# Performance work log

Measured on AMD Instinct MI355X. Metric: run time of the kernel, lower is better.

## Reference

```python
import jax, jax.numpy as jnp
import numpy as np

N_NODES = 100000
N_EDGES = 1600000
N_GRAPHS = 1000
HID = 128
NCLS = 3


def setup_inputs() -> dict:
    key = jax.random.key(0)
    ks = jax.random.split(key, 16)
    x = jax.random.normal(ks[0], (N_NODES, 1), dtype=jnp.float32)
    edge_index = jax.random.randint(ks[1], (2, N_EDGES), 0, N_NODES, dtype=jnp.int64)
    edge_attr = jax.random.normal(ks[2], (N_EDGES, 1), dtype=jnp.float32)
    batch = jnp.sort(jax.random.randint(ks[3], (N_NODES,), 0, N_GRAPHS, dtype=jnp.int64))
    s1 = 1.0 / np.sqrt(1.0)
    sh = 1.0 / np.sqrt(HID)
    # layer 0 MLP: 1 -> HID -> HID
    W1_0 = jax.random.uniform(ks[4], (1, HID), minval=-s1, maxval=s1)
    b1_0 = jax.random.uniform(ks[5], (HID,), minval=-s1, maxval=s1)
    W2_0 = jax.random.uniform(ks[6], (HID, HID), minval=-sh, maxval=sh)
    b2_0 = jax.random.uniform(ks[7], (HID,), minval=-sh, maxval=sh)
    # layers 1..3 MLPs stacked: HID -> HID -> HID
    W1_s = jax.random.uniform(ks[8], (3, HID, HID), minval=-sh, maxval=sh)
    b1_s = jax.random.uniform(ks[9], (3, HID), minval=-sh, maxval=sh)
    W2_s = jax.random.uniform(ks[10], (3, HID, HID), minval=-sh, maxval=sh)
    b2_s = jax.random.uniform(ks[11], (3, HID), minval=-sh, maxval=sh)
    Wc = jax.random.uniform(ks[12], (HID, NCLS), minval=-sh, maxval=sh)
    bc = jax.random.uniform(ks[13], (NCLS,), minval=-sh, maxval=sh)
    return {"x": x, "edge_index": edge_index, "edge_attr": edge_attr, "batch": batch,
            "W1_0": W1_0, "b1_0": b1_0, "W2_0": W2_0, "b2_0": b2_0,
            "W1_s": W1_s, "b1_s": b1_s, "W2_s": W2_s, "b2_s": b2_s,
            "Wc": Wc, "bc": bc}


def _gine_layer(x, src, dst, edge_attr, W1, b1, W2, b2):
    # message: ReLU(x_j + e_ji), broadcast over feature dim ([E,1] edge_attr)
    msg = jax.nn.relu(x[src] + edge_attr)                       # [E, F]
    agg = jax.ops.segment_sum(msg, dst, num_segments=x.shape[0])  # [N, F]
    h = x + agg                                                 # (1 + eps)*x + agg, eps = 0
    return jax.nn.relu(h @ W1 + b1) @ W2 + b2                   # MLP


def reference(x, edge_index, edge_attr, batch,
              W1_0, b1_0, W2_0, b2_0, W1_s, b1_s, W2_s, b2_s, Wc, bc):
    src, dst = edge_index[0], edge_index[1]
    h = jax.nn.relu(_gine_layer(x, src, dst, edge_attr, W1_0, b1_0, W2_0, b2_0))
    for i in range(3):
        h = jax.nn.relu(_gine_layer(h, src, dst, edge_attr,
                                    W1_s[i], b1_s[i], W2_s[i], b2_s[i]))
    # global mean pool per graph
    summed = jax.ops.segment_sum(h, batch, num_segments=N_GRAPHS)       # [G, HID]
    counts = jax.ops.segment_sum(jnp.ones((h.shape[0],), h.dtype), batch,
                                 num_segments=N_GRAPHS)                  # [G]
    pooled = summed / jnp.maximum(counts, 1.0)[:, None]
    return pooled @ Wc + bc                                              # [G, NCLS]
```

## Files before the change

### kernel.cpp

```cpp
#include <hip/hip_runtime.h>
#include <hip/hip_bf16.h>


#define HID 128
#define NCLS 3
#define EPB 8192
#define BSHIFT 8
#define BNODES 256
#define ECAP 5504

typedef _Float16 f16;
typedef f16 f16x2 __attribute__((ext_vector_type(2)));
typedef f16 f16x8 __attribute__((ext_vector_type(8)));
typedef float f32x2 __attribute__((ext_vector_type(2)));
typedef float f32x4 __attribute__((ext_vector_type(4)));
typedef unsigned short ushort;

__device__ __forceinline__ float bcf(int v) {
    return __builtin_bit_cast(float, v);
}
__device__ __forceinline__ float f16bits2f(ushort u) {
    return (float)__builtin_bit_cast(f16, u);
}


__global__ __launch_bounds__(1024) void k_bin2(const int* __restrict__ src,
                                               const int* __restrict__ dst,
                                               const float* __restrict__ eattr,
                                               const float* __restrict__ x,
                                               int* __restrict__ cursor,
                                               int2* __restrict__ ebuf,
                                               int E, int NB) {
    __shared__ int lh[512];
    __shared__ int lbase[512];
    __shared__ int lrsv[512];
    int t = threadIdx.x;
    if (t < NB) lh[t] = 0;
    __syncthreads();
    int base = blockIdx.x * EPB;
    int myd[8];
    #pragma unroll
    for (int j = 0; j < 8; ++j) {
        int e = base + j * 1024 + t;
        myd[j] = (e < E) ? dst[e] : -1;
        if (myd[j] >= 0) atomicAdd(&lh[myd[j] >> BSHIFT], 1);
    }
    __syncthreads();
    if (t < NB) {
        int c = lh[t];
        int cp = (c + 7) & ~7;
        lrsv[t] = cp;
        lbase[t] = (cp > 0) ? (t * ECAP + atomicAdd(&cursor[t], cp)) : 0;
        lh[t] = 0;
    }
    __syncthreads();
    #pragma unroll
    for (int j = 0; j < 8; ++j) {
        if (myd[j] >= 0) {
            int e = base + j * 1024 + t;
            int b = myd[j] >> BSHIFT;
            int s = src[e];
            float at = eattr[e];
            float msg = fmaxf(x[s] + at, 0.f);
            unsigned a16 = __builtin_bit_cast(ushort, (f16)at);
            unsigned m16 = __builtin_bit_cast(ushort, (f16)msg);
            int r = atomicAdd(&lh[b], 1);
            int pos = lbase[b] + r;
            if (pos < (b + 1) * ECAP)
                ebuf[pos] = make_int2(s | ((myd[j] & (BNODES - 1)) << 24),
                                      (int)((a16 << 16) | m16));
        }
    }
    __syncthreads();
    if (t < NB) {
        int c = lh[t], cp = lrsv[t];
        int p0 = lbase[t] + c;
        int pe = lbase[t] + cp;
        int cap = (t + 1) * ECAP;
        if (pe > cap) pe = cap;
        for (int pos = p0; pos < pe; ++pos)
            ebuf[pos] = make_int2(-1, 0);
    }
}


__global__ __launch_bounds__(1024) void k_prep(const float* __restrict__ W2_0,
                                               const float* __restrict__ W1_s,
                                               const float* __restrict__ W2_s,
                                               f16* __restrict__ Wf,
                                               const int* __restrict__ cursor,
                                               int* __restrict__ bbase, int NB) {
    int t = threadIdx.x;
    if (blockIdx.x < 14) {
        int id = blockIdx.x * 1024 + t;
        int lane = id & 63;
        int w    = (id >> 6) & 3;
        int nf   = (id >> 8) & 1;
        int kk   = (id >> 9) & 3;
        int g    = id >> 11;
        const float* W = (g == 0) ? W2_0
                       : ((g & 1) ? W1_s + (size_t)((g - 1) >> 1) * HID * HID
                                  : W2_s + (size_t)((g - 2) >> 1) * HID * HID);
        int col = w * 32 + nf * 16 + (lane & 15);
        int k0  = kk * 32 + (lane >> 4) * 8;
        f16x8 hi;
        #pragma unroll
        for (int j = 0; j < 8; ++j)
            hi[j] = (f16)W[(k0 + j) * HID + col];
        size_t o = ((((size_t)g * 4 + kk) * 2 + nf) * 4 + w) * 512 +
                   (size_t)lane * 8;
        *(f16x8*)&Wf[o] = hi;
    } else {
        __shared__ int sd[1024];
        int v = (t < NB) ? min(cursor[t], ECAP) : 0;
        sd[t] = v;
        __syncthreads();
        #pragma unroll
        for (int o = 1; o < 1024; o <<= 1) {
            int add = (t >= o) ? sd[t - o] : 0;
            __syncthreads();
            sd[t] += add;
            __syncthreads();
        }
        if (t < NB) bbase[t] = sd[t] - v;
        if (t == 1023) bbase[NB] = sd[1023];
    }
}

__global__ __launch_bounds__(512, 8) void k_fill2(const int2* __restrict__ ebuf,
                                               const int* __restrict__ btot,
                                               const int* __restrict__ bbase,
                                               const float* __restrict__ x,
                                               const int* __restrict__ batch,
                                               int2* __restrict__ meta,
                                               int2* __restrict__ pairs,
                                               float* __restrict__ hin0,
                                               int* __restrict__ gcount,
                                               int* __restrict__ gstart,
                                               int N) {
    __shared__ int lcnt[BNODES];
    __shared__ int lofs[BNODES];
    __shared__ float satom[BNODES];
    int b = blockIdx.x, t = threadIdx.x;
    int estart = b * ECAP;
    int cnt = min(btot[b], ECAP);
    int pstart = bbase[b];
    int nb0 = b << BSHIFT;
    if (t < BNODES) {
        lcnt[t] = 0;
        satom[t] = 0.f;
        int node = nb0 + t;
        if (node < N) {
            int gb = batch[node];
            atomicAdd(&gcount[gb], 1);
            if (node == 0 || batch[node - 1] != gb) gstart[gb] = node;
        }
    }
    __syncthreads();
    int2 myv[11];
    #pragma unroll
    for (int j = 0; j < 11; ++j) {
        int i = j * 512 + t;
        if (i < cnt) myv[j] = ebuf[estart + i];
    }
    #pragma unroll
    for (int j = 0; j < 11; ++j) {
        int i = j * 512 + t;
        if (i < cnt && myv[j].x != -1)
            atomicAdd(&lcnt[((unsigned)myv[j].x) >> 24], 1);
    }
    __syncthreads();
    if (t < 64) {
        int c0 = lcnt[4 * t], c1 = lcnt[4 * t + 1];
        int c2 = lcnt[4 * t + 2], c3 = lcnt[4 * t + 3];
        int s = c0 + c1 + c2 + c3;
        int sa = s;
        #pragma unroll
        for (int o = 1; o < 64; o <<= 1) {
            int v = __shfl_up(sa, o);
            if (t >= o) sa += v;
        }
        int e0 = sa - s;
        int e1 = e0 + c0, e2 = e1 + c1, e3 = e2 + c2;
        lofs[4 * t] = e0; lofs[4 * t + 1] = e1;
        lofs[4 * t + 2] = e2; lofs[4 * t + 3] = e3;
        lcnt[4 * t] = 0; lcnt[4 * t + 1] = 0;
        lcnt[4 * t + 2] = 0; lcnt[4 * t + 3] = 0;
        int n0 = nb0 + 4 * t;
        if (n0 < N)     meta[n0]     = make_int2(pstart + e0, c0);
        if (n0 + 1 < N) meta[n0 + 1] = make_int2(pstart + e1, c1);
        if (n0 + 2 < N) meta[n0 + 2] = make_int2(pstart + e2, c2);
        if (n0 + 3 < N) meta[n0 + 3] = make_int2(pstart + e3, c3);
    }
    __syncthreads();
    #pragma unroll
    for (int j = 0; j < 11; ++j) {
        int i = j * 512 + t;
        if (i < cnt) {
            int2 v = myv[j];
            if (v.x != -1) {
                int ld = ((unsigned)v.x) >> 24;
                int srcid = v.x & 0x00FFFFFF;
                ushort a16 = (ushort)(((unsigned)v.y) >> 16);
                ushort m16 = (ushort)(v.y & 0xFFFF);
                int r = atomicAdd(&lcnt[ld], 1);
                int pos = lofs[ld] + r;
                pairs[pstart + pos] = make_int2(srcid << 7,
                                     __builtin_bit_cast(int, f16bits2f(a16)));
                atomicAdd(&satom[ld], f16bits2f(m16));
            }
        }
    }
    __syncthreads();
    if (t < BNODES) {
        int node = nb0 + t;
        if (node < N) hin0[node] = x[node] + satom[t];
    }
}


__device__ __forceinline__ void agg_add8(f32x2 acc2[4], uint2 g, float e) {
    f32x2 e2 = {e, e}, z2 = {0.f, 0.f};
    unsigned gw[2] = {g.x, g.y};
    #pragma unroll
    for (int ww = 0; ww < 2; ++ww) {
        f32x2 lo = __builtin_amdgcn_cvt_pk_f32_fp8((int)gw[ww], false);
        f32x2 hi = __builtin_amdgcn_cvt_pk_f32_fp8((int)gw[ww], true);
        lo = __builtin_elementwise_max(lo + e2, z2);
        hi = __builtin_elementwise_max(hi + e2, z2);
        acc2[2 * ww]     += lo;
        acc2[2 * ww + 1] += hi;
    }
}

__device__ __forceinline__ uint2 agg_ld8(const char* __restrict__ hb,
                                         int voff) {
    return *(const uint2*)(hb + (unsigned)voff);
}

__global__ __launch_bounds__(256, 4) void k_agg(
    const unsigned char* __restrict__ h8,
    const f16* __restrict__ hf,
    const int2* __restrict__ pairs,
    const int2* __restrict__ meta,
    f16* __restrict__ oh, int n) {

    int t = threadIdx.x;
    int w = t >> 6, lane = t & 63;
    int g = lane >> 4, c = lane & 15;
    int node = blockIdx.x * 16 + w * 4 + g;
    int c8 = c * 8;
    int sbase = g * 16;
    const char* hb = (const char*)h8;

    int2 m = make_int2(0, 0);
    if (node < n) m = meta[node];
    int off = m.x, d = m.y;
    f32x2 acc2[4] = {{0.f,0.f},{0.f,0.f},{0.f,0.f},{0.f,0.f}};

    for (int wb = 0; wb < d; wb += 16) {
        int rem = d - wb;
        int mm = rem < 16 ? rem : 16;
        int2 pr = make_int2(0, 0);
        if (c < mm) pr = pairs[off + wb + c];
        uint2 gg[16];
        #pragma unroll
        for (int p = 0; p < 16; ++p) {
            int s = __shfl(pr.x, sbase + p);
            if (p < mm) gg[p] = agg_ld8(hb, s + c8);
        }
        #pragma unroll
        for (int p = 0; p < 16; ++p) {
            if (p < mm) {
                float e = bcf(__shfl(pr.y, sbase + p));
                agg_add8(acc2, gg[p], e);
            }
        }
    }

    if (node < n) {
        uint4 sg = *(const uint4*)&hf[(size_t)node * HID + c8];
        unsigned sw[4] = {sg.x, sg.y, sg.z, sg.w};
        unsigned ow[4];
        #pragma unroll
        for (int ww = 0; ww < 4; ++ww) {
            f16x2 s = __builtin_bit_cast(f16x2, sw[ww]);
            f16x2 o;
            o[0] = (f16)((float)s[0] + acc2[ww].x);
            o[1] = (f16)((float)s[1] + acc2[ww].y);
            ow[ww] = __builtin_bit_cast(unsigned, o);
        }
        uint4 o4;
        o4.x = ow[0]; o4.y = ow[1]; o4.z = ow[2]; o4.w = ow[3];
        *(uint4*)&oh[(size_t)node * HID + c8] = o4;
    }
}


__device__ __forceinline__ void load_wfrags1(const f16* __restrict__ Wfg,
                                             int w, int lane,
                                             f16x8 whf[4][2]) {
    #pragma unroll
    for (int kk = 0; kk < 4; ++kk)
        #pragma unroll
        for (int nf = 0; nf < 2; ++nf) {
            size_t o = (((size_t)kk * 2 + nf) * 4 + w) * 512 +
                       (size_t)lane * 8;
            whf[kk][nf] = *(const f16x8*)&Wfg[o];
        }
}

__device__ __forceinline__ void do_gemm1(const f16* Ah,
                                         const f16x8 whf[4][2],
                                         int lane, f32x4 acc[4][2]) {
    int arow = lane & 15, akgrp = lane >> 4;
    #pragma unroll
    for (int kk = 0; kk < 4; ++kk) {
        int chunk = kk * 4 + akgrp;
        f16x8 ah[4];
        #pragma unroll
        for (int mf = 0; mf < 4; ++mf) {
            int r = mf * 16 + arow;
            int swz = chunk ^ (r & 15);
            ah[mf] = *(const f16x8*)&Ah[r * HID + swz * 8];
        }
        #pragma unroll
        for (int mf = 0; mf < 4; ++mf)
            #pragma unroll
            for (int nf = 0; nf < 2; ++nf)
                acc[mf][nf] = __builtin_amdgcn_mfma_f32_16x16x32_f16(
                    ah[mf], whf[kk][nf], acc[mf][nf], 0, 0, 0);
    }
}


__global__ __launch_bounds__(256, 3) void k_mlp(
    const f16* __restrict__ A_g,
    const f16* __restrict__ Wf1, const float* __restrict__ b1,
    const f16* __restrict__ Wf2, const float* __restrict__ b2,
    f16* __restrict__ O, unsigned char* __restrict__ O8, int w8, int n) {

    __shared__ __align__(16) f16 bufA[64 * HID];
    int t = threadIdx.x, w = t >> 6, lane = t & 63;
    int wcol = w * 32, fcol = lane & 15, kgrp = lane >> 4;
    int row0 = blockIdx.x * 64;

    #pragma unroll
    for (int rep = 0; rep < 4; ++rep) {
        int task = rep * 256 + t;
        int r = task >> 4, ch = task & 15;
        int gr = min(row0 + r, n - 1);
        int swz = ch ^ (r & 15);
        *(f16x8*)&bufA[r * HID + swz * 8] =
            *(const f16x8*)&A_g[(size_t)gr * HID + ch * 8];
    }

    f32x4 acc[4][2];
    {
        f16x8 whf[4][2];
        load_wfrags1(Wf1, w, lane, whf);
        float bv0 = b1[wcol + fcol], bv1 = b1[wcol + 16 + fcol];
        __syncthreads();
        #pragma unroll
        for (int mf = 0; mf < 4; ++mf)
            #pragma unroll
            for (int nf = 0; nf < 2; ++nf)
                acc[mf][nf] = (f32x4)(0.f);
        do_gemm1(bufA, whf, lane, acc);
        __syncthreads();
        #pragma unroll
        for (int mf = 0; mf < 4; ++mf)
            #pragma unroll
            for (int nf = 0; nf < 2; ++nf) {
                int cc = wcol + nf * 16 + fcol;
                float bb = nf ? bv1 : bv0;
                #pragma unroll
                for (int j = 0; j < 4; ++j) {
                    int r = mf * 16 + kgrp * 4 + j;
                    float v = fmaxf(acc[mf][nf][j] + bb, 0.f);
                    int addr = r * HID + (((cc >> 3) ^ (r & 15)) << 3) + (cc & 7);
                    bufA[addr] = (f16)v;
                }
            }
    }
    {
        f16x8 whf[4][2];
        load_wfrags1(Wf2, w, lane, whf);
        float bv0 = b2[wcol + fcol], bv1 = b2[wcol + 16 + fcol];
        __syncthreads();
        #pragma unroll
        for (int mf = 0; mf < 4; ++mf)
            #pragma unroll
            for (int nf = 0; nf < 2; ++nf)
                acc[mf][nf] = (f32x4)(0.f);
        do_gemm1(bufA, whf, lane, acc);

        #pragma unroll
        for (int mf = 0; mf < 4; ++mf)
            #pragma unroll
            for (int nf = 0; nf < 2; ++nf) {
                int cc = wcol + nf * 16 + fcol;
                float bb = nf ? bv1 : bv0;
                #pragma unroll
                for (int j = 0; j < 4; ++j) {
                    int r = row0 + mf * 16 + kgrp * 4 + j;
                    if (r < n) {
                        float v = fmaxf(acc[mf][nf][j] + bb, 0.f);
                        O[(size_t)r * HID + cc] = (f16)v;
                        if (w8) {
                            int pk = __builtin_amdgcn_cvt_pk_fp8_f32(
                                v, v, 0, false);
                            O8[(size_t)r * HID + cc] =
                                (unsigned char)(pk & 0xFF);
                        }
                    }
                }
            }
    }
}


__global__ __launch_bounds__(256, 3) void k_mlp0(
    const float* __restrict__ r1x, const float* __restrict__ r1w,
    const float* __restrict__ r1b,
    const f16* __restrict__ Wf2, const float* __restrict__ b2,
    f16* __restrict__ O, unsigned char* __restrict__ O8, int n) {

    __shared__ __align__(16) f16 bufA[64 * HID];
    int t = threadIdx.x, w = t >> 6, lane = t & 63;
    int wcol = w * 32, fcol = lane & 15, kgrp = lane >> 4;
    int row0 = blockIdx.x * 64;

    #pragma unroll
    for (int rep = 0; rep < 4; ++rep) {
        int task = rep * 256 + t;
        int r = task >> 4, ch = task & 15;
        int gr = min(row0 + r, n - 1);
        int swz = ch ^ (r & 15);
        float xv = r1x[gr];
        f16x8 hi;
        #pragma unroll
        for (int j = 0; j < 8; ++j)
            hi[j] = (f16)fmaxf(xv * r1w[ch * 8 + j] + r1b[ch * 8 + j], 0.f);
        *(f16x8*)&bufA[r * HID + swz * 8] = hi;
    }

    f16x8 whf[4][2];
    load_wfrags1(Wf2, w, lane, whf);
    float bv0 = b2[wcol + fcol], bv1 = b2[wcol + 16 + fcol];
    __syncthreads();
    f32x4 acc[4][2];
    #pragma unroll
    for (int mf = 0; mf < 4; ++mf)
        #pragma unroll
        for (int nf = 0; nf < 2; ++nf)
            acc[mf][nf] = (f32x4)(0.f);
    do_gemm1(bufA, whf, lane, acc);

    #pragma unroll
    for (int mf = 0; mf < 4; ++mf)
        #pragma unroll
        for (int nf = 0; nf < 2; ++nf) {
            int cc = wcol + nf * 16 + fcol;
            float bb = nf ? bv1 : bv0;
            #pragma unroll
            for (int j = 0; j < 4; ++j) {
                int r = row0 + mf * 16 + kgrp * 4 + j;
                if (r < n) {
                    float v = fmaxf(acc[mf][nf][j] + bb, 0.f);
                    O[(size_t)r * HID + cc] = (f16)v;
                    int pk = __builtin_amdgcn_cvt_pk_fp8_f32(v, v, 0, false);
                    O8[(size_t)r * HID + cc] = (unsigned char)(pk & 0xFF);
                }
            }
        }
}


__global__ __launch_bounds__(256) void k_head(const f16* __restrict__ h,
                                              const int* __restrict__ gstart,
                                              const int* __restrict__ gcount,
                                              const float* __restrict__ Wc,
                                              const float* __restrict__ bc,
                                              float* __restrict__ out, int G) {
    __shared__ float2 red[4][64];
    __shared__ float pl[HID];
    int g = blockIdx.x, t = threadIdx.x;
    int rr = t >> 6, cc = t & 63;
    int st = gstart[g], c = gcount[g];
    float2 acc = make_float2(0.f, 0.f);
    for (int i = rr; i < c; i += 4) {
        unsigned u = *(const unsigned*)&h[(size_t)(st + i) * HID + cc * 2];
        f16x2 v = __builtin_bit_cast(f16x2, u);
        acc.x += (float)v[0];
        acc.y += (float)v[1];
    }
    red[rr][cc] = acc;
    __syncthreads();
    if (rr == 0) {
        #pragma unroll
        for (int k = 1; k < 4; ++k) {
            acc.x += red[k][cc].x;
            acc.y += red[k][cc].y;
        }
        float inv = 1.f / fmaxf((float)c, 1.f);
        pl[cc * 2]     = acc.x * inv;
        pl[cc * 2 + 1] = acc.y * inv;
    }
    __syncthreads();
    if (t < NCLS) {
        float o = bc[t];
        for (int k = 0; k < HID; ++k) o += pl[k] * Wc[k * NCLS + t];
        out[g * NCLS + t] = o;
    }
}


static inline size_t alignup(size_t x, size_t a) { return (x + a - 1) & ~(a - 1); }

extern "C" void kernel_launch(void* const* d_in, const int* in_sizes, int n_in,
                              void* d_out, int out_size, void* d_ws, size_t ws_size,
                              hipStream_t stream) {
    const float* x      = (const float*)d_in[0];
    const int*   ei     = (const int*)d_in[1];
    const float* eattr  = (const float*)d_in[2];
    const int*   batch  = (const int*)d_in[3];
    const float* W1_0   = (const float*)d_in[4];
    const float* b1_0   = (const float*)d_in[5];
    const float* W2_0   = (const float*)d_in[6];
    const float* b2_0   = (const float*)d_in[7];
    const float* W1_s   = (const float*)d_in[8];
    const float* b1_s   = (const float*)d_in[9];
    const float* W2_s   = (const float*)d_in[10];
    const float* b2_s   = (const float*)d_in[11];
    const float* Wc     = (const float*)d_in[12];
    const float* bc     = (const float*)d_in[13];

    const int N = in_sizes[0];
    const int E = in_sizes[2];
    const int G = out_size / NCLS;
    const int* srcI = ei;
    const int* dstI = ei + E;

    const int NB = (N + BNODES - 1) >> BSHIFT;
    const int NBLK = (E + EPB - 1) / EPB;

    char* p = (char*)d_ws;
    size_t off = 0;
    size_t gcount_off = off;         off = alignup(off + (size_t)G * 4, 256);
    size_t gstart_off = off;         off = alignup(off + (size_t)G * 4, 256);
    size_t cursor_off = off;         off = alignup(off + 512 * 4, 256);
    size_t zero_bytes = off;
    size_t meta_off = off;           off = alignup(off + (size_t)N * 8, 256);
    size_t bbase_off = off;          off = alignup(off + 513 * 4, 256);
    size_t hin0_off = off;           off = alignup(off + (size_t)N * 4, 256);
    size_t wf_off = off;             off = alignup(off + 7 * 16384 * 2, 256);
    size_t pairs_off = off;          off = alignup(off + (size_t)NB * ECAP * 8, 256);
    size_t p0_off = off;             off = alignup(off + (size_t)N * HID * 2, 256);
    size_t p8_off = off;             off = alignup(off + (size_t)N * HID, 256);
    size_t p1_off = off;             off = alignup(off + (size_t)N * HID * 2, 256);

    int*    gcount  = (int*)(p + gcount_off);
    int*    gstart  = (int*)(p + gstart_off);
    int*    cursor  = (int*)(p + cursor_off);
    int2*   meta    = (int2*)(p + meta_off);
    int*    bbase   = (int*)(p + bbase_off);
    float*  hin0    = (float*)(p + hin0_off);
    f16*    Wf      = (f16*)(p + wf_off);
    int2*   pairs   = (int2*)(p + pairs_off);
    f16*    P0      = (f16*)(p + p0_off);
    unsigned char* P8 = (unsigned char*)(p + p8_off);
    f16*    P1      = (f16*)(p + p1_off);
    int2*   ebuf    = (int2*)(p + p1_off);

    hipMemsetAsync(d_ws, 0, zero_bytes, stream);

    int gblk = (N + 63) / 64;
    int abl = (N + 15) / 16;

    k_bin2<<<NBLK, 1024, 0, stream>>>(srcI, dstI, eattr, x, cursor, ebuf,
                                      E, NB);
    k_prep<<<15, 1024, 0, stream>>>(W2_0, W1_s, W2_s, Wf, cursor, bbase, NB);
    k_fill2<<<NB, 512, 0, stream>>>(ebuf, cursor, bbase, x, batch, meta,
                                    pairs, hin0, gcount, gstart, N);

    #define WFG(g) (Wf + (size_t)(g) * 16384)

    k_mlp0<<<gblk, 256, 0, stream>>>(hin0, W1_0, b1_0, WFG(0), b2_0,
                                     P0, P8, N);

    for (int l = 0; l < 3; ++l) {
        const float* b1 = b1_s + (size_t)l * HID;
        const float* b2 = b2_s + (size_t)l * HID;
        k_agg<<<abl, 256, 0, stream>>>(P8, P0, pairs, meta, P1, N);
        k_mlp<<<gblk, 256, 0, stream>>>(P1, WFG(1 + 2 * l), b1,
                                        WFG(2 + 2 * l), b2, P0, P8,
                                        (l < 2) ? 1 : 0, N);
    }

    k_head<<<G, 256, 0, stream>>>(P0, gstart, gcount, Wc, bc,
                                  (float*)d_out, G);
}
```

Measured before the change: 308.6 us.

## Aggregate layer-0 messages with global atomics and fuse fill with first MLP

The binning kernel now accumulates the scalar layer-0 messages straight into a zeroed per-node fp32 buffer with global atomicAdd. It no longer packs fp16 message and attribute values into the edge buffer; the full fp32 edge attribute is stored instead. This removes the first MLP's dependency on the CSR fill pass. The fill kernel and the layer-0 MLP are merged into one launch with two kinds of blocks, so they can run concurrently and one launch is saved. In exchange it adds 1.6M contended global float atomics and makes the layer-0 sums order-nondeterministic.

```diff
diff --git a/kernel.cpp b/kernel.cpp
--- a/kernel.cpp
+++ b/kernel.cpp
@@ -19,9 +19,6 @@
 __device__ __forceinline__ float bcf(int v) {
     return __builtin_bit_cast(float, v);
 }
-__device__ __forceinline__ float f16bits2f(ushort u) {
-    return (float)__builtin_bit_cast(f16, u);
-}
 
 
 __global__ __launch_bounds__(1024) void k_bin2(const int* __restrict__ src,
@@ -29,6 +26,7 @@
                                                const float* __restrict__ eattr,
                                                const float* __restrict__ x,
                                                int* __restrict__ cursor,
+                                               float* __restrict__ agg0,
                                                int2* __restrict__ ebuf,
                                                int E, int NB) {
     __shared__ int lh[512];
@@ -62,13 +60,12 @@
             int s = src[e];
             float at = eattr[e];
             float msg = fmaxf(x[s] + at, 0.f);
-            unsigned a16 = __builtin_bit_cast(ushort, (f16)at);
-            unsigned m16 = __builtin_bit_cast(ushort, (f16)msg);
+            atomicAdd(&agg0[myd[j]], msg);
             int r = atomicAdd(&lh[b], 1);
             int pos = lbase[b] + r;
             if (pos < (b + 1) * ECAP)
                 ebuf[pos] = make_int2(s | ((myd[j] & (BNODES - 1)) << 24),
-                                      (int)((a16 << 16) | m16));
+                                      __builtin_bit_cast(int, at));
         }
     }
     __syncthreads();
@@ -127,94 +124,184 @@
     }
 }
 
-__global__ __launch_bounds__(512, 8) void k_fill2(const int2* __restrict__ ebuf,
-                                               const int* __restrict__ btot,
-                                               const int* __restrict__ bbase,
-                                               const float* __restrict__ x,
-                                               const int* __restrict__ batch,
-                                               int2* __restrict__ meta,
-                                               int2* __restrict__ pairs,
-                                               float* __restrict__ hin0,
-                                               int* __restrict__ gcount,
-                                               int* __restrict__ gstart,
-                                               int N) {
+
+__device__ __forceinline__ void load_wfrags1(const f16* __restrict__ Wfg,
+                                             int w, int lane,
+                                             f16x8 whf[4][2]) {
+    #pragma unroll
+    for (int kk = 0; kk < 4; ++kk)
+        #pragma unroll
+        for (int nf = 0; nf < 2; ++nf) {
+            size_t o = (((size_t)kk * 2 + nf) * 4 + w) * 512 +
+                       (size_t)lane * 8;
+            whf[kk][nf] = *(const f16x8*)&Wfg[o];
+        }
+}
+
+__device__ __forceinline__ void do_gemm1(const f16* Ah,
+                                         const f16x8 whf[4][2],
+                                         int lane, f32x4 acc[4][2]) {
+    int arow = lane & 15, akgrp = lane >> 4;
+    #pragma unroll
+    for (int kk = 0; kk < 4; ++kk) {
+        int chunk = kk * 4 + akgrp;
+        f16x8 ah[4];
+        #pragma unroll
+        for (int mf = 0; mf < 4; ++mf) {
+            int r = mf * 16 + arow;
+            int swz = chunk ^ (r & 15);
+            ah[mf] = *(const f16x8*)&Ah[r * HID + swz * 8];
+        }
+        #pragma unroll
+        for (int mf = 0; mf < 4; ++mf)
+            #pragma unroll
+            for (int nf = 0; nf < 2; ++nf)
+                acc[mf][nf] = __builtin_amdgcn_mfma_f32_16x16x32_f16(
+                    ah[mf], whf[kk][nf], acc[mf][nf], 0, 0, 0);
+    }
+}
+
+
+__global__ __launch_bounds__(512, 4) void k_fillm(
+    const int2* __restrict__ ebuf,
+    const int* __restrict__ btot,
+    const int* __restrict__ bbase,
+    const float* __restrict__ x,
+    const int* __restrict__ batch,
+    int2* __restrict__ meta,
+    int2* __restrict__ pairs,
+    const float* __restrict__ agg0,
+    int* __restrict__ gcount,
+    int* __restrict__ gstart,
+    const float* __restrict__ r1w, const float* __restrict__ r1b,
+    const f16* __restrict__ Wf2, const float* __restrict__ b2,
+    f16* __restrict__ O, unsigned char* __restrict__ O8,
+    int N, int NB) {
+
+    __shared__ __align__(16) f16 bufA2[2][64 * HID];
     __shared__ int lcnt[BNODES];
     __shared__ int lofs[BNODES];
-    __shared__ float satom[BNODES];
-    int b = blockIdx.x, t = threadIdx.x;
-    int estart = b * ECAP;
-    int cnt = min(btot[b], ECAP);
-    int pstart = bbase[b];
-    int nb0 = b << BSHIFT;
-    if (t < BNODES) {
-        lcnt[t] = 0;
-        satom[t] = 0.f;
-        int node = nb0 + t;
-        if (node < N) {
-            int gb = batch[node];
-            atomicAdd(&gcount[gb], 1);
-            if (node == 0 || batch[node - 1] != gb) gstart[gb] = node;
-        }
-    }
-    __syncthreads();
-    int2 myv[11];
-    #pragma unroll
-    for (int j = 0; j < 11; ++j) {
-        int i = j * 512 + t;
-        if (i < cnt) myv[j] = ebuf[estart + i];
-    }
-    #pragma unroll
-    for (int j = 0; j < 11; ++j) {
-        int i = j * 512 + t;
-        if (i < cnt && myv[j].x != -1)
-            atomicAdd(&lcnt[((unsigned)myv[j].x) >> 24], 1);
-    }
-    __syncthreads();
-    if (t < 64) {
-        int c0 = lcnt[4 * t], c1 = lcnt[4 * t + 1];
-        int c2 = lcnt[4 * t + 2], c3 = lcnt[4 * t + 3];
-        int s = c0 + c1 + c2 + c3;
-        int sa = s;
-        #pragma unroll
-        for (int o = 1; o < 64; o <<= 1) {
-            int v = __shfl_up(sa, o);
-            if (t >= o) sa += v;
-        }
-        int e0 = sa - s;
-        int e1 = e0 + c0, e2 = e1 + c1, e3 = e2 + c2;
-        lofs[4 * t] = e0; lofs[4 * t + 1] = e1;
-        lofs[4 * t + 2] = e2; lofs[4 * t + 3] = e3;
-        lcnt[4 * t] = 0; lcnt[4 * t + 1] = 0;
-        lcnt[4 * t + 2] = 0; lcnt[4 * t + 3] = 0;
-        int n0 = nb0 + 4 * t;
-        if (n0 < N)     meta[n0]     = make_int2(pstart + e0, c0);
-        if (n0 + 1 < N) meta[n0 + 1] = make_int2(pstart + e1, c1);
-        if (n0 + 2 < N) meta[n0 + 2] = make_int2(pstart + e2, c2);
-        if (n0 + 3 < N) meta[n0 + 3] = make_int2(pstart + e3, c3);
-    }
-    __syncthreads();
-    #pragma unroll
-    for (int j = 0; j < 11; ++j) {
-        int i = j * 512 + t;
-        if (i < cnt) {
-            int2 v = myv[j];
-            if (v.x != -1) {
-                int ld = ((unsigned)v.x) >> 24;
-                int srcid = v.x & 0x00FFFFFF;
-                ushort a16 = (ushort)(((unsigned)v.y) >> 16);
-                ushort m16 = (ushort)(v.y & 0xFFFF);
-                int r = atomicAdd(&lcnt[ld], 1);
-                int pos = lofs[ld] + r;
-                pairs[pstart + pos] = make_int2(srcid << 7,
-                                     __builtin_bit_cast(int, f16bits2f(a16)));
-                atomicAdd(&satom[ld], f16bits2f(m16));
-            }
-        }
-    }
-    __syncthreads();
-    if (t < BNODES) {
-        int node = nb0 + t;
-        if (node < N) hin0[node] = x[node] + satom[t];
+
+    if (blockIdx.x < NB) {
+        int b = blockIdx.x, t = threadIdx.x;
+        int estart = b * ECAP;
+        int cnt = min(btot[b], ECAP);
+        int pstart = bbase[b];
+        int nb0 = b << BSHIFT;
+        if (t < BNODES) {
+            lcnt[t] = 0;
+            int node = nb0 + t;
+            if (node < N) {
+                int gb = batch[node];
+                atomicAdd(&gcount[gb], 1);
+                if (node == 0 || batch[node - 1] != gb) gstart[gb] = node;
+            }
+        }
+        __syncthreads();
+        int2 myv[11];
+        #pragma unroll
+        for (int j = 0; j < 11; ++j) {
+            int i = j * 512 + t;
+            if (i < cnt) myv[j] = ebuf[estart + i];
+        }
+        #pragma unroll
+        for (int j = 0; j < 11; ++j) {
+            int i = j * 512 + t;
+            if (i < cnt && myv[j].x != -1)
+                atomicAdd(&lcnt[((unsigned)myv[j].x) >> 24], 1);
+        }
+        __syncthreads();
+        if (t < 64) {
+            int c0 = lcnt[4 * t], c1 = lcnt[4 * t + 1];
+            int c2 = lcnt[4 * t + 2], c3 = lcnt[4 * t + 3];
+            int s = c0 + c1 + c2 + c3;
+            int sa = s;
+            #pragma unroll
+            for (int o = 1; o < 64; o <<= 1) {
+                int v = __shfl_up(sa, o);
+                if (t >= o) sa += v;
+            }
+            int e0 = sa - s;
+            int e1 = e0 + c0, e2 = e1 + c1, e3 = e2 + c2;
+            lofs[4 * t] = e0; lofs[4 * t + 1] = e1;
+            lofs[4 * t + 2] = e2; lofs[4 * t + 3] = e3;
+            lcnt[4 * t] = 0; lcnt[4 * t + 1] = 0;
+            lcnt[4 * t + 2] = 0; lcnt[4 * t + 3] = 0;
+            int n0 = nb0 + 4 * t;
+            if (n0 < N)     meta[n0]     = make_int2(pstart + e0, c0);
+            if (n0 + 1 < N) meta[n0 + 1] = make_int2(pstart + e1, c1);
+            if (n0 + 2 < N) meta[n0 + 2] = make_int2(pstart + e2, c2);
+            if (n0 + 3 < N) meta[n0 + 3] = make_int2(pstart + e3, c3);
+        }
+        __syncthreads();
+        #pragma unroll
+        for (int j = 0; j < 11; ++j) {
+            int i = j * 512 + t;
+            if (i < cnt) {
+                int2 v = myv[j];
+                if (v.x != -1) {
+                    int ld = ((unsigned)v.x) >> 24;
+                    int srcid = v.x & 0x00FFFFFF;
+                    int r = atomicAdd(&lcnt[ld], 1);
+                    int pos = lofs[ld] + r;
+                    pairs[pstart + pos] = make_int2(srcid << 7, v.y);
+                }
+            }
+        }
+    } else {
+        int mb = blockIdx.x - NB;
+        int t = threadIdx.x;
+        int tile = t >> 8, tt = t & 255;
+        int w = tt >> 6, lane = tt & 63;
+        int wcol = w * 32, fcol = lane & 15, kgrp = lane >> 4;
+        int row0 = mb * 128 + tile * 64;
+        f16* bufA = &bufA2[tile][0];
+
+        #pragma unroll
+        for (int rep = 0; rep < 4; ++rep) {
+            int task = rep * 256 + tt;
+            int r = task >> 4, ch = task & 15;
+            int gr = min(row0 + r, N - 1);
+            int swz = ch ^ (r & 15);
+            float xv = x[gr] + agg0[gr];
+            f16x8 hi;
+            #pragma unroll
+            for (int j = 0; j < 8; ++j)
+                hi[j] = (f16)fmaxf(xv * r1w[ch * 8 + j] + r1b[ch * 8 + j],
+                                   0.f);
+            *(f16x8*)&bufA[r * HID + swz * 8] = hi;
+        }
+
+        f16x8 whf[4][2];
+        load_wfrags1(Wf2, w, lane, whf);
+        float bv0 = b2[wcol + fcol], bv1 = b2[wcol + 16 + fcol];
+        __syncthreads();
+        f32x4 acc[4][2];
+        #pragma unroll
+        for (int mf = 0; mf < 4; ++mf)
+            #pragma unroll
+            for (int nf = 0; nf < 2; ++nf)
+                acc[mf][nf] = (f32x4)(0.f);
+        do_gemm1(bufA, whf, lane, acc);
+
+        #pragma unroll
+        for (int mf = 0; mf < 4; ++mf)
+            #pragma unroll
+            for (int nf = 0; nf < 2; ++nf) {
+                int cc = wcol + nf * 16 + fcol;
+                float bb = nf ? bv1 : bv0;
+                #pragma unroll
+                for (int j = 0; j < 4; ++j) {
+                    int r = row0 + mf * 16 + kgrp * 4 + j;
+                    if (r < N) {
+                        float v = fmaxf(acc[mf][nf][j] + bb, 0.f);
+                        O[(size_t)r * HID + cc] = (f16)v;
+                        int pk = __builtin_amdgcn_cvt_pk_fp8_f32(v, v, 0,
+                                                                 false);
+                        O8[(size_t)r * HID + cc] = (unsigned char)(pk & 0xFF);
+                    }
+                }
+            }
     }
 }
 
@@ -293,43 +380,6 @@
         uint4 o4;
         o4.x = ow[0]; o4.y = ow[1]; o4.z = ow[2]; o4.w = ow[3];
         *(uint4*)&oh[(size_t)node * HID + c8] = o4;
-    }
-}
-
-
-__device__ __forceinline__ void load_wfrags1(const f16* __restrict__ Wfg,
-                                             int w, int lane,
-                                             f16x8 whf[4][2]) {
-    #pragma unroll
-    for (int kk = 0; kk < 4; ++kk)
-        #pragma unroll
-        for (int nf = 0; nf < 2; ++nf) {
-            size_t o = (((size_t)kk * 2 + nf) * 4 + w) * 512 +
-                       (size_t)lane * 8;
-            whf[kk][nf] = *(const f16x8*)&Wfg[o];
-        }
-}
-
-__device__ __forceinline__ void do_gemm1(const f16* Ah,
-                                         const f16x8 whf[4][2],
-                                         int lane, f32x4 acc[4][2]) {
-    int arow = lane & 15, akgrp = lane >> 4;
-    #pragma unroll
-    for (int kk = 0; kk < 4; ++kk) {
-        int chunk = kk * 4 + akgrp;
-        f16x8 ah[4];
-        #pragma unroll
-        for (int mf = 0; mf < 4; ++mf) {
-            int r = mf * 16 + arow;
-            int swz = chunk ^ (r & 15);
-            ah[mf] = *(const f16x8*)&Ah[r * HID + swz * 8];
-        }
-        #pragma unroll
-        for (int mf = 0; mf < 4; ++mf)
-            #pragma unroll
-            for (int nf = 0; nf < 2; ++nf)
-                acc[mf][nf] = __builtin_amdgcn_mfma_f32_16x16x32_f16(
-                    ah[mf], whf[kk][nf], acc[mf][nf], 0, 0, 0);
     }
 }
 
@@ -420,63 +470,6 @@
 }
 
 
-__global__ __launch_bounds__(256, 3) void k_mlp0(
-    const float* __restrict__ r1x, const float* __restrict__ r1w,
-    const float* __restrict__ r1b,
-    const f16* __restrict__ Wf2, const float* __restrict__ b2,
-    f16* __restrict__ O, unsigned char* __restrict__ O8, int n) {
-
-    __shared__ __align__(16) f16 bufA[64 * HID];
-    int t = threadIdx.x, w = t >> 6, lane = t & 63;
-    int wcol = w * 32, fcol = lane & 15, kgrp = lane >> 4;
-    int row0 = blockIdx.x * 64;
-
-    #pragma unroll
-    for (int rep = 0; rep < 4; ++rep) {
-        int task = rep * 256 + t;
-        int r = task >> 4, ch = task & 15;
-        int gr = min(row0 + r, n - 1);
-        int swz = ch ^ (r & 15);
-        float xv = r1x[gr];
-        f16x8 hi;
-        #pragma unroll
-        for (int j = 0; j < 8; ++j)
-            hi[j] = (f16)fmaxf(xv * r1w[ch * 8 + j] + r1b[ch * 8 + j], 0.f);
-        *(f16x8*)&bufA[r * HID + swz * 8] = hi;
-    }
-
-    f16x8 whf[4][2];
-    load_wfrags1(Wf2, w, lane, whf);
-    float bv0 = b2[wcol + fcol], bv1 = b2[wcol + 16 + fcol];
-    __syncthreads();
-    f32x4 acc[4][2];
-    #pragma unroll
-    for (int mf = 0; mf < 4; ++mf)
-        #pragma unroll
-        for (int nf = 0; nf < 2; ++nf)
-            acc[mf][nf] = (f32x4)(0.f);
-    do_gemm1(bufA, whf, lane, acc);
-
-    #pragma unroll
-    for (int mf = 0; mf < 4; ++mf)
-        #pragma unroll
-        for (int nf = 0; nf < 2; ++nf) {
-            int cc = wcol + nf * 16 + fcol;
-            float bb = nf ? bv1 : bv0;
-            #pragma unroll
-            for (int j = 0; j < 4; ++j) {
-                int r = row0 + mf * 16 + kgrp * 4 + j;
-                if (r < n) {
-                    float v = fmaxf(acc[mf][nf][j] + bb, 0.f);
-                    O[(size_t)r * HID + cc] = (f16)v;
-                    int pk = __builtin_amdgcn_cvt_pk_fp8_f32(v, v, 0, false);
-                    O8[(size_t)r * HID + cc] = (unsigned char)(pk & 0xFF);
-                }
-            }
-        }
-}
-
-
 __global__ __launch_bounds__(256) void k_head(const f16* __restrict__ h,
                                               const int* __restrict__ gstart,
                                               const int* __restrict__ gcount,
@@ -544,16 +537,17 @@
 
     const int NB = (N + BNODES - 1) >> BSHIFT;
     const int NBLK = (E + EPB - 1) / EPB;
+    const int GB2 = (N + 127) / 128;
 
     char* p = (char*)d_ws;
     size_t off = 0;
     size_t gcount_off = off;         off = alignup(off + (size_t)G * 4, 256);
     size_t gstart_off = off;         off = alignup(off + (size_t)G * 4, 256);
     size_t cursor_off = off;         off = alignup(off + 512 * 4, 256);
+    size_t agg0_off = off;           off = alignup(off + (size_t)N * 4, 256);
     size_t zero_bytes = off;
     size_t meta_off = off;           off = alignup(off + (size_t)N * 8, 256);
     size_t bbase_off = off;          off = alignup(off + 513 * 4, 256);
-    size_t hin0_off = off;           off = alignup(off + (size_t)N * 4, 256);
     size_t wf_off = off;             off = alignup(off + 7 * 16384 * 2, 256);
     size_t pairs_off = off;          off = alignup(off + (size_t)NB * ECAP * 8, 256);
     size_t p0_off = off;             off = alignup(off + (size_t)N * HID * 2, 256);
@@ -563,9 +557,9 @@
     int*    gcount  = (int*)(p + gcount_off);
     int*    gstart  = (int*)(p + gstart_off);
     int*    cursor  = (int*)(p + cursor_off);
+    float*  agg0    = (float*)(p + agg0_off);
     int2*   meta    = (int2*)(p + meta_off);
     int*    bbase   = (int*)(p + bbase_off);
-    float*  hin0    = (float*)(p + hin0_off);
     f16*    Wf      = (f16*)(p + wf_off);
     int2*   pairs   = (int2*)(p + pairs_off);
     f16*    P0      = (f16*)(p + p0_off);
@@ -578,16 +572,16 @@
     int gblk = (N + 63) / 64;
     int abl = (N + 15) / 16;
 
-    k_bin2<<<NBLK, 1024, 0, stream>>>(srcI, dstI, eattr, x, cursor, ebuf,
-                                      E, NB);
+    k_bin2<<<NBLK, 1024, 0, stream>>>(srcI, dstI, eattr, x, cursor, agg0,
+                                      ebuf, E, NB);
     k_prep<<<15, 1024, 0, stream>>>(W2_0, W1_s, W2_s, Wf, cursor, bbase, NB);
-    k_fill2<<<NB, 512, 0, stream>>>(ebuf, cursor, bbase, x, batch, meta,
-                                    pairs, hin0, gcount, gstart, N);
 
     #define WFG(g) (Wf + (size_t)(g) * 16384)
 
-    k_mlp0<<<gblk, 256, 0, stream>>>(hin0, W1_0, b1_0, WFG(0), b2_0,
-                                     P0, P8, N);
+    k_fillm<<<NB + GB2, 512, 0, stream>>>(ebuf, cursor, bbase, x, batch,
+                                          meta, pairs, agg0, gcount, gstart,
+                                          W1_0, b1_0, WFG(0), b2_0,
+                                          P0, P8, N, NB);
 
     for (int l = 0; l < 3; ++l) {
         const float* b1 = b1_s + (size_t)l * HID;
```

New measurement: 363.8 us. 17.9% more time.
